# Optimization experiments

Hardware: AMD Instinct MI355X
Metric: run time of the kernel (lower is better)

Reference implementation:

```python
import jax, jax.numpy as jnp
import numpy as np

B, T, D, K, M, TOPK = 16, 2048, 512, 8192, 3, 8


def setup_inputs() -> dict:
    key = jax.random.key(0)
    k1, k2, k3 = jax.random.split(key, 3)
    return {
        "query": jax.random.normal(k1, (B, T, D), dtype=jnp.float32),
        "completeness": jax.random.uniform(k2, (B,), dtype=jnp.float32),
        "codebook": jax.random.normal(k3, (M, K, D), dtype=jnp.float32),
        "log_temperature": jnp.log(jnp.float32(0.07)),
        "modality_idx": 0,
        "top_k": TOPK,
    }


def reference(query, completeness, codebook, log_temperature, modality_idx, top_k):
    b, t, d = query.shape
    n = b * t
    cb = jax.lax.stop_gradient(codebook[modality_idx])  # [K, D], detached in original
    k_codes = cb.shape[0]

    q = query.reshape(n, d)
    # squared euclidean distances via ||q||^2 + ||c||^2 - 2 q c^T  -> [N, K]
    dist_sq = (q * q).sum(-1, keepdims=True) + (cb * cb).sum(-1) - 2.0 * (q @ cb.T)
    sim = -dist_sq / np.float32(np.sqrt(d))

    temperature = jnp.exp(log_temperature)
    comp = jnp.repeat(completeness, t)[:, None]          # [N, 1]
    adaptive_temp = temperature * (2.0 - comp)           # [N, 1]

    topk_sim, topk_idx = jax.lax.top_k(sim, top_k)       # [N, k]
    topk_w = jax.nn.softmax(topk_sim / adaptive_temp, axis=-1)  # [N, k]

    topk_cb = cb[topk_idx]                               # [N, k, D] gather
    retrieved = (topk_w[..., None] * topk_cb).sum(-2)    # [N, D]

    rows = jnp.arange(n)[:, None]
    retrieval_weights = jnp.zeros((n, k_codes), q.dtype).at[rows, topk_idx].set(topk_w)

    return retrieved.reshape(b, t, d), retrieval_weights.reshape(b, t, k_codes)
```

## Files before the change

kernel.cpp:

```cpp
#include <hip/hip_runtime.h>
#include <math.h>

#define NB 16
#define NT 2048
#define ND 512
#define NK 8192
#define NN (NB*NT)
#define NTOP 8
#define SCALE_SIM 0.044194173824159216f

#define CHUNK 2048
#define CT 128
#define BK 32

typedef __attribute__((ext_vector_type(8))) short bf16x8;
typedef __attribute__((ext_vector_type(4))) float f32x4;

__device__ __forceinline__ unsigned int f2bf(float f) {
  unsigned int u = __float_as_uint(f);
  return (u + 0x7FFFu + ((u >> 16) & 1u)) >> 16;
}

__device__ __forceinline__ void gl16(const void* g, void* l) {
  __builtin_amdgcn_global_load_lds((const __attribute__((address_space(1))) void*)g,
                                   (__attribute__((address_space(3))) void*)l, 16, 0, 0);
}

__device__ __forceinline__ unsigned sortable(float f) {
  unsigned fb = __float_as_uint(f);
  unsigned sx = (unsigned)((int)fb >> 31);
  return fb ^ (sx | 0x80000000u);
}

__global__ void prep_kernel(const float* __restrict__ q,
                            const float* __restrict__ cbbase,
                            const int* __restrict__ modality,
                            ushort* __restrict__ q_bf, ushort* __restrict__ cb_bf,
                            float* __restrict__ cc) {
  int gw = (blockIdx.x * blockDim.x + threadIdx.x) >> 6;
  int lane = threadIdx.x & 63;
  if (gw < NN) {
    const float* src = q + (size_t)gw * ND + lane * 8;
    float4 v0 = ((const float4*)src)[0];
    float4 v1 = ((const float4*)src)[1];
    uint4 o;
    o.x = f2bf(v0.x) | (f2bf(v0.y) << 16);
    o.y = f2bf(v0.z) | (f2bf(v0.w) << 16);
    o.z = f2bf(v1.x) | (f2bf(v1.y) << 16);
    o.w = f2bf(v1.z) | (f2bf(v1.w) << 16);
    *(uint4*)(q_bf + (size_t)gw * ND + lane * 8) = o;
  } else {
    int r = gw - NN;
    const float* cb = cbbase + (size_t)(*modality) * ((size_t)NK * ND);
    const float* src = cb + (size_t)r * ND + lane * 8;
    float4 v0 = ((const float4*)src)[0];
    float4 v1 = ((const float4*)src)[1];
    uint4 o;
    o.x = f2bf(v0.x) | (f2bf(v0.y) << 16);
    o.y = f2bf(v0.z) | (f2bf(v0.w) << 16);
    o.z = f2bf(v1.x) | (f2bf(v1.y) << 16);
    o.w = f2bf(v1.z) | (f2bf(v1.w) << 16);
    *(uint4*)(cb_bf + (size_t)r * ND + lane * 8) = o;
    float s = 0.f;
    s = fmaf(v0.x, v0.x, s); s = fmaf(v0.y, v0.y, s);
    s = fmaf(v0.z, v0.z, s); s = fmaf(v0.w, v0.w, s);
    s = fmaf(v1.x, v1.x, s); s = fmaf(v1.y, v1.y, s);
    s = fmaf(v1.z, v1.z, s); s = fmaf(v1.w, v1.w, s);
#pragma unroll
    for (int off = 32; off > 0; off >>= 1) s += __shfl_down(s, off);
    if (lane == 0) cc[r] = s;
  }
}

__global__ __launch_bounds__(256, 2)
void sim_topk_kernel(const ushort* __restrict__ q_bf, const ushort* __restrict__ cb_bf,
                     const float* __restrict__ cc,
                     unsigned* __restrict__ cand) {
  __shared__ ushort A_lds[2][128 * 32];
  __shared__ ushort B_lds[2][128 * 32];
  __shared__ __align__(16) float cc_lds[CHUNK];
  unsigned (*mg)[64][12] = reinterpret_cast<unsigned (*)[64][12]>(&A_lds[0][0]);

  const int rb = blockIdx.x & 255, ch = blockIdx.x >> 8;
  const int r0 = rb * 128, ccol0 = ch * CHUNK;
  const int t = threadIdx.x, lane = t & 63, w = t >> 6;
  const int wr = w >> 1, wc = w & 1;
  const int m = lane & 15, quad = lane >> 4;

  {
    const f32x4* src = (const f32x4*)(cc + ccol0);
    *(f32x4*)&cc_lds[t * 8]     = src[t * 2];
    *(f32x4*)&cc_lds[t * 8 + 4] = src[t * 2 + 1];
  }

  const int sl = ((lane & 3) ^ ((lane >> 3) & 3)) * 8;
  const ushort* gA = q_bf + (size_t)(r0 + w * 32 + (lane >> 2)) * ND + sl;
  const ushort* gB = cb_bf + (size_t)(ccol0 + w * 32 + (lane >> 2)) * ND + sl;

  const int swq = quad ^ ((m >> 1) & 3);
  const int aoff = (wr * 64 + m) * 32 + swq * 8;
  const int boff = (wc * 64 + m) * 32 + swq * 8;

  unsigned tl[4][12];
#pragma unroll
  for (int j = 0; j < 4; ++j)
#pragma unroll
    for (int s = 0; s < 12; ++s) tl[j][s] = 0u;

  {
    ushort* lA = &A_lds[0][w * 1024];
    ushort* lB = &B_lds[0][w * 1024];
    gl16(gA, lA);
    gl16(gA + 16 * ND, lA + 512);
    gl16(gB, lB);
    gl16(gB + 16 * ND, lB + 512);
  }

  for (int tile = 0; tile < 16; ++tile) {
    f32x4 acc[4][4];
#pragma unroll
    for (int i = 0; i < 4; ++i)
#pragma unroll
      for (int j = 0; j < 4; ++j) acc[i][j] = (f32x4){0.f, 0.f, 0.f, 0.f};

#pragma unroll
    for (int s = 0; s < ND / BK; ++s) {
      __syncthreads();
      {
        int ntile = (s < 15) ? tile : tile + 1;
        if (ntile < 16) {
          int ns = (s + 1) & 15;
          int nb = (s + 1) & 1;
          ushort* lA = &A_lds[nb][w * 1024];
          ushort* lB = &B_lds[nb][w * 1024];
          const ushort* gBt = gB + (size_t)ntile * CT * ND;
          gl16(gA + ns * 32, lA);
          gl16(gA + ns * 32 + 16 * ND, lA + 512);
          gl16(gBt + ns * 32, lB);
          gl16(gBt + ns * 32 + 16 * ND, lB + 512);
        }
      }
      const ushort* Ab = &A_lds[s & 1][0];
      const ushort* Bb = &B_lds[s & 1][0];
      bf16x8 a[4], b[4];
#pragma unroll
      for (int j = 0; j < 4; ++j) a[j] = *(const bf16x8*)&Ab[aoff + j * 512];
#pragma unroll
      for (int i = 0; i < 4; ++i) b[i] = *(const bf16x8*)&Bb[boff + i * 512];
#pragma unroll
      for (int i = 0; i < 4; ++i)
#pragma unroll
        for (int j = 0; j < 4; ++j)
          acc[i][j] = __builtin_amdgcn_mfma_f32_16x16x32_bf16(b[i], a[j], acc[i][j], 0, 0, 0);
    }

    const int cb0 = tile * CT + wc * 64 + quad * 4;
    const int invb = 2047 - cb0;
#pragma unroll
    for (int i = 0; i < 4; ++i) {
      f32x4 cq = *(const f32x4*)&cc_lds[cb0 + i * 16];
#pragma unroll
      for (int r = 0; r < 4; ++r) {
#pragma unroll
        for (int j = 0; j < 4; ++j) {
          float key = fmaf(2.f, acc[i][j][r], -cq[r]);
          unsigned c = (sortable(key) & 0xFFFFF800u) | (unsigned)(invb - (i * 16 + r));
#pragma unroll
          for (int s2 = 0; s2 < 12; ++s2) {
            unsigned hi = tl[j][s2] > c ? tl[j][s2] : c;
            unsigned lo = tl[j][s2] > c ? c : tl[j][s2];
            tl[j][s2] = hi; c = lo;
          }
        }
      }
    }
  }

#pragma unroll
  for (int j = 0; j < 4; ++j) {
    __syncthreads();
#pragma unroll
    for (int s = 0; s < 12; ++s) mg[w][lane][s] = tl[j][s];
    __syncthreads();
    if (wc == 0 && lane < 16) {
      unsigned t16[16];
#pragma unroll
      for (int s = 0; s < 16; ++s) t16[s] = 0u;
#pragma unroll 1
      for (int h = 0; h < 2; ++h) {
#pragma unroll 1
        for (int q = 0; q < 4; ++q) {
#pragma unroll 1
          for (int s = 0; s < 12; ++s) {
            unsigned c = mg[wr * 2 + h][q * 16 + lane][s];
#pragma unroll
            for (int s2 = 0; s2 < 16; ++s2) {
              unsigned hi = t16[s2] > c ? t16[s2] : c;
              unsigned lo = t16[s2] > c ? c : t16[s2];
              t16[s2] = hi; c = lo;
            }
          }
        }
      }
      size_t base = (size_t)(r0 + wr * 64 + j * 16 + lane) * 64 + ch * 16;
#pragma unroll
      for (int s = 0; s < 16; ++s) cand[base + s] = t16[s];
    }
  }
}

__global__ __launch_bounds__(256, 3)
void finalize_kernel(const float* __restrict__ q, const float* __restrict__ comp,
                     const float* __restrict__ cbbase, const float* __restrict__ logtemp,
                     const int* __restrict__ modality, const float* __restrict__ cc,
                     const unsigned* __restrict__ cand,
                     float* __restrict__ out_r, float* __restrict__ out_w) {
  __shared__ int ssel[4][12];
  const int w = threadIdx.x >> 6, lane = threadIdx.x & 63;
  const int r = blockIdx.x * 4 + w;
  const float* cb = cbbase + (size_t)(*modality) * ((size_t)NK * ND);

  unsigned u = cand[(size_t)r * 64 + lane];
  unsigned kp = u >> 11;
  int ci = ((lane >> 4) << 11) + (2047 - (int)(u & 0x7FFu));
  int rank = 0;
  for (int j = 0; j < 64; ++j) {
    unsigned kj = (unsigned)__builtin_amdgcn_readlane((int)kp, j);
    int cj = (int)__builtin_amdgcn_readlane(ci, j);
    rank += (kj > kp || (kj == kp && cj < ci)) ? 1 : 0;
  }
  if (rank < 12) ssel[w][rank] = ci;
  __syncthreads();

  int i12[12];
#pragma unroll
  for (int j = 0; j < 12; ++j) i12[j] = ssel[w][j];

  const float4* qv = (const float4*)(q + (size_t)r * ND);
  float4 q0 = qv[lane], q1 = qv[lane + 64];
  float4 c0[12], c1[12];
  float k12[12];
#pragma unroll
  for (int j = 0; j < 12; ++j) {
    const float4* cp = (const float4*)(cb + (size_t)i12[j] * ND);
    c0[j] = cp[lane]; c1[j] = cp[lane + 64];
    float d = 0.f;
    d = fmaf(q0.x, c0[j].x, d); d = fmaf(q0.y, c0[j].y, d);
    d = fmaf(q0.z, c0[j].z, d); d = fmaf(q0.w, c0[j].w, d);
    d = fmaf(q1.x, c1[j].x, d); d = fmaf(q1.y, c1[j].y, d);
    d = fmaf(q1.z, c1[j].z, d); d = fmaf(q1.w, c1[j].w, d);
    k12[j] = d;
  }
#pragma unroll
  for (int j = 0; j < 12; ++j) {
    float d = k12[j];
#pragma unroll
    for (int off = 32; off > 0; off >>= 1) d += __shfl_xor(d, off);
    k12[j] = fmaf(2.f, d, -cc[i12[j]]);
  }

  float key = -INFINITY; int cidx = 0x7fffffff;
#pragma unroll
  for (int j = 0; j < 12; ++j) {
    key  = (lane == j) ? k12[j] : key;
    cidx = (lane == j) ? i12[j] : cidx;
  }
  int rk = 0;
#pragma unroll
  for (int j = 0; j < 12; ++j)
    rk += (k12[j] > key || (k12[j] == key && i12[j] < cidx)) ? 1 : 0;
  bool sel = (lane < 12) && (rk < NTOP);

  float at = __expf(*logtemp) * (2.f - comp[r >> 11]);
  float mx = k12[0];
#pragma unroll
  for (int j = 1; j < 12; ++j) mx = fmaxf(mx, k12[j]);
  float e = sel ? __expf((key - mx) * (SCALE_SIM / at)) : 0.f;
  float es = e;
#pragma unroll
  for (int off = 32; off > 0; off >>= 1) es += __shfl_xor(es, off);
  float wgt = e / es;
  if (sel) out_w[(size_t)r * NK + cidx] = wgt;

  float w12[12];
#pragma unroll
  for (int j = 0; j < 12; ++j) w12[j] = __shfl(wgt, j);

  float4 a0 = make_float4(0.f, 0.f, 0.f, 0.f), a1 = a0;
#pragma unroll
  for (int j = 0; j < 12; ++j) {
    float ww = w12[j];
    a0.x = fmaf(ww, c0[j].x, a0.x); a0.y = fmaf(ww, c0[j].y, a0.y);
    a0.z = fmaf(ww, c0[j].z, a0.z); a0.w = fmaf(ww, c0[j].w, a0.w);
    a1.x = fmaf(ww, c1[j].x, a1.x); a1.y = fmaf(ww, c1[j].y, a1.y);
    a1.z = fmaf(ww, c1[j].z, a1.z); a1.w = fmaf(ww, c1[j].w, a1.w);
  }
  float4* orp = (float4*)(out_r + (size_t)r * ND);
  orp[lane] = a0; orp[lane + 64] = a1;
}

extern "C" void kernel_launch(void* const* d_in, const int* in_sizes, int n_in,
                              void* d_out, int out_size, void* d_ws, size_t ws_size,
                              hipStream_t stream) {
  (void)in_sizes; (void)n_in; (void)out_size; (void)ws_size;
  const float* q        = (const float*)d_in[0];
  const float* comp     = (const float*)d_in[1];
  const float* cbbase   = (const float*)d_in[2];
  const float* logtemp  = (const float*)d_in[3];
  const int*   modality = (const int*)d_in[4];

  float* out_r = (float*)d_out;
  float* out_w = out_r + (size_t)NN * ND;

  ushort*   q_bf  = (ushort*)d_ws;
  ushort*   cb_bf = q_bf + (size_t)NN * ND;
  float*    ccw   = (float*)(cb_bf + (size_t)NK * ND);
  unsigned* cand  = (unsigned*)(ccw + NK);

  prep_kernel<<<dim3((NN + NK) / 4), dim3(256), 0, stream>>>(q, cbbase, modality, q_bf, cb_bf, ccw);
  sim_topk_kernel<<<dim3((NN / 128) * 4), dim3(256), 0, stream>>>(q_bf, cb_bf, ccw, cand);
  finalize_kernel<<<dim3(NN / 4), dim3(256), 0, stream>>>(q, comp, cbbase, logtemp, modality, ccw,
                                                          cand, out_r, out_w);
}
```

Measured before the change: 1.670 ms.

## Triple-buffer LDS tiles with prefetch distance two and explicit vmcnt waits

Moves the GEMM main loop from double to triple LDS buffering: two K-slices are prefetched up front and each step issues the load two slices ahead into a rotating stage buffer. The full __syncthreads is replaced by a partial s_waitcnt vmcnt(4) plus a raw s_barrier, so the newest loads can stay in flight while older ones are consumed. The aim is to hide more global-to-LDS latency behind MFMA work. The cost is 16 KB more LDS per block, which may limit occupancy at 2 blocks per CU, and the hand-placed waitcnt makes correctness depend on the exact order in which loads are issued.

```diff
diff --git a/kernel.cpp b/kernel.cpp
--- a/kernel.cpp
+++ b/kernel.cpp
@@ -76,8 +76,8 @@
 void sim_topk_kernel(const ushort* __restrict__ q_bf, const ushort* __restrict__ cb_bf,
                      const float* __restrict__ cc,
                      unsigned* __restrict__ cand) {
-  __shared__ ushort A_lds[2][128 * 32];
-  __shared__ ushort B_lds[2][128 * 32];
+  __shared__ ushort A_lds[3][128 * 32];
+  __shared__ ushort B_lds[3][128 * 32];
   __shared__ __align__(16) float cc_lds[CHUNK];
   unsigned (*mg)[64][12] = reinterpret_cast<unsigned (*)[64][12]>(&A_lds[0][0]);
 
@@ -107,14 +107,21 @@
 #pragma unroll
     for (int s = 0; s < 12; ++s) tl[j][s] = 0u;
 
+  __syncthreads();
+
   {
-    ushort* lA = &A_lds[0][w * 1024];
-    ushort* lB = &B_lds[0][w * 1024];
-    gl16(gA, lA);
-    gl16(gA + 16 * ND, lA + 512);
-    gl16(gB, lB);
-    gl16(gB + 16 * ND, lB + 512);
-  }
+    gl16(gA,                &A_lds[0][w * 1024]);
+    gl16(gA + 16 * ND,      &A_lds[0][w * 1024 + 512]);
+    gl16(gB,                &B_lds[0][w * 1024]);
+    gl16(gB + 16 * ND,      &B_lds[0][w * 1024 + 512]);
+    gl16(gA + 32,           &A_lds[1][w * 1024]);
+    gl16(gA + 32 + 16 * ND, &A_lds[1][w * 1024 + 512]);
+    gl16(gB + 32,           &B_lds[1][w * 1024]);
+    gl16(gB + 32 + 16 * ND, &B_lds[1][w * 1024 + 512]);
+  }
+
+  ushort *rdA = &A_lds[0][0], *nxA = &A_lds[1][0], *stA = &A_lds[2][0];
+  ushort *rdB = &B_lds[0][0], *nxB = &B_lds[1][0], *stB = &B_lds[2][0];
 
   for (int tile = 0; tile < 16; ++tile) {
     f32x4 acc[4][4];
@@ -124,34 +131,40 @@
       for (int j = 0; j < 4; ++j) acc[i][j] = (f32x4){0.f, 0.f, 0.f, 0.f};
 
 #pragma unroll
-    for (int s = 0; s < ND / BK; ++s) {
-      __syncthreads();
+    for (int s = 0; s < 16; ++s) {
+      if (tile == 15 && s == 15) {
+        asm volatile("s_waitcnt vmcnt(0)" ::: "memory");
+      } else {
+        asm volatile("s_waitcnt vmcnt(4)" ::: "memory");
+      }
+      __builtin_amdgcn_s_barrier();
+      __builtin_amdgcn_sched_barrier(0);
+
       {
-        int ntile = (s < 15) ? tile : tile + 1;
+        int ntile = (s < 14) ? tile : tile + 1;
         if (ntile < 16) {
-          int ns = (s + 1) & 15;
-          int nb = (s + 1) & 1;
-          ushort* lA = &A_lds[nb][w * 1024];
-          ushort* lB = &B_lds[nb][w * 1024];
+          int ns = (s + 2) & 15;
           const ushort* gBt = gB + (size_t)ntile * CT * ND;
-          gl16(gA + ns * 32, lA);
-          gl16(gA + ns * 32 + 16 * ND, lA + 512);
-          gl16(gBt + ns * 32, lB);
-          gl16(gBt + ns * 32 + 16 * ND, lB + 512);
+          gl16(gA + ns * 32,            stA + w * 1024);
+          gl16(gA + ns * 32 + 16 * ND,  stA + w * 1024 + 512);
+          gl16(gBt + ns * 32,           stB + w * 1024);
+          gl16(gBt + ns * 32 + 16 * ND, stB + w * 1024 + 512);
         }
       }
-      const ushort* Ab = &A_lds[s & 1][0];
-      const ushort* Bb = &B_lds[s & 1][0];
+
       bf16x8 a[4], b[4];
 #pragma unroll
-      for (int j = 0; j < 4; ++j) a[j] = *(const bf16x8*)&Ab[aoff + j * 512];
-#pragma unroll
-      for (int i = 0; i < 4; ++i) b[i] = *(const bf16x8*)&Bb[boff + i * 512];
+      for (int j = 0; j < 4; ++j) a[j] = *(const bf16x8*)&rdA[aoff + j * 512];
+#pragma unroll
+      for (int i = 0; i < 4; ++i) b[i] = *(const bf16x8*)&rdB[boff + i * 512];
 #pragma unroll
       for (int i = 0; i < 4; ++i)
 #pragma unroll
         for (int j = 0; j < 4; ++j)
           acc[i][j] = __builtin_amdgcn_mfma_f32_16x16x32_bf16(b[i], a[j], acc[i][j], 0, 0, 0);
+
+      ushort* t1 = stA; stA = rdA; rdA = nxA; nxA = t1;
+      ushort* t2 = stB; stB = rdB; rdB = nxB; nxB = t2;
     }
 
     const int cb0 = tile * CT + wc * 64 + quad * 4;
```

New measurement: 1.631 ms. 2.3% less time.
